# Kernel tuning notes

Measured on AMD Instinct MI355X. Metric: run time of the kernel, lower is better.

## Reference

```python
import jax, jax.numpy as jnp
import numpy as np

N_NODES = 50000
N_REL = 8
IN_DIM = 128
HID = 128
N_EDGES = 800000
N_TRIP = 100000


def setup_inputs() -> dict:
    key = jax.random.key(0)
    ks = jax.random.split(key, 12)
    s = 0.05
    return {
        "emb": jax.random.normal(ks[0], (N_NODES, IN_DIM), jnp.float32),
        "W0": jax.random.normal(ks[1], (N_REL, IN_DIM, HID), jnp.float32) * s,
        "root0": jax.random.normal(ks[2], (IN_DIM, HID), jnp.float32) * s,
        "b0": jnp.zeros((HID,), jnp.float32),
        "W1": jax.random.normal(ks[3], (N_REL, HID, HID), jnp.float32) * s,
        "root1": jax.random.normal(ks[4], (HID, HID), jnp.float32) * s,
        "b1": jnp.zeros((HID,), jnp.float32),
        "rel_emb": jax.random.normal(ks[5], (N_REL, HID), jnp.float32),
        "edge_index": jax.random.randint(ks[6], (2, N_EDGES), 0, N_NODES, jnp.int64 if jax.config.read('jax_enable_x64') else jnp.int32),
        "edge_type": jax.random.randint(ks[7], (N_EDGES,), 0, N_REL, jnp.int32),
        "head_idx": jax.random.randint(ks[8], (N_TRIP,), 0, N_NODES, jnp.int32),
        "rel_idx": jax.random.randint(ks[9], (N_TRIP,), 0, N_REL, jnp.int32),
        "tail_idx": jax.random.randint(ks[10], (N_TRIP,), 0, N_NODES, jnp.int32),
    }


def _rgcn_layer(h, W, root, bias, src, dst, edge_type):
    # PyG RGCNConv: per-relation MEAN aggregation of neighbor features at dst,
    # transformed by the relation weight, plus root transform and bias.
    # Mean commutes with the linear map, so aggregate raw features first.
    n, r = N_NODES, N_REL
    seg = dst * r + edge_type  # (E,) joint (dst, relation) segment id
    msg = h[src]               # (E, d) irregular gather
    sums = jax.ops.segment_sum(msg, seg, num_segments=n * r)          # (N*R, d)
    cnt = jax.ops.segment_sum(jnp.ones((src.shape[0],), h.dtype), seg,
                              num_segments=n * r)                     # (N*R,)
    mean = (sums / jnp.maximum(cnt, 1.0)[:, None]).reshape(n, r, -1)  # (N, R, d)
    return jnp.einsum('nrd,rdh->nh', mean, W) + h @ root + bias


def reference(emb, W0, root0, b0, W1, root1, b1, rel_emb,
              edge_index, edge_type, head_idx, rel_idx, tail_idx):
    src = edge_index[0]
    dst = edge_index[1]
    et = edge_type.astype(jnp.int32)
    h = emb
    h = jax.nn.relu(_rgcn_layer(h, W0, root0, b0, src, dst, et))
    h = jax.nn.relu(_rgcn_layer(h, W1, root1, b1, src, dst, et))
    # DistMult score: sum(h_head * r * h_tail)
    score = jnp.sum(h[head_idx] * rel_emb[rel_idx] * h[tail_idx], axis=-1)
    return score
```

## Files before the change

### kernel.cpp

```cpp
#include <hip/hip_runtime.h>
#include <hip/hip_bf16.h>

#define N_NODES 50000
#define N_REL   8
#define DIM     128
#define N_EDGES 800000
#define N_TRIP  100000
#define NDBLK   196
#define NB2     (N_REL * NDBLK)
#define CAP2    1024
#define NOFF    (N_REL * N_NODES + 1)

typedef __attribute__((ext_vector_type(8))) short bf16x8;
typedef __attribute__((ext_vector_type(4))) float f32x4;

static __device__ __forceinline__ unsigned short f2b(float f) {
    __hip_bfloat16 h = __float2bfloat16(f);
    return *reinterpret_cast<unsigned short*>(&h);
}
static __device__ __forceinline__ float blo(unsigned int u) {
    return __uint_as_float(u << 16);
}
static __device__ __forceinline__ float bhi(unsigned int u) {
    return __uint_as_float(u & 0xffff0000u);
}
static __device__ __forceinline__ int lds_off(int row, int chunk) {
    return (row * 16 + (chunk ^ (row & 7))) * 8;
}

__global__ __launch_bounds__(256) void bucket_scatter(
        const int* __restrict__ edge_index,
        const int* __restrict__ edge_type,
        int* __restrict__ gcnt,
        unsigned int* __restrict__ slack) {
    __shared__ int hist[NB2];
    __shared__ int cur[NB2];
    int tid = threadIdx.x;
    for (int i = tid; i < NB2; i += 256) hist[i] = 0;
    __syncthreads();
    int base = blockIdx.x * 4096;
    unsigned int w[16];
    int bk[16];
    #pragma unroll
    for (int i = 0; i < 16; ++i) {
        int e = base + i * 256 + tid;
        if (e < N_EDGES) {
            int src = edge_index[e];
            int dst = edge_index[N_EDGES + e];
            int r = edge_type[e];
            w[i] = (unsigned int)src | ((unsigned int)(dst & 255) << 16);
            bk[i] = r * NDBLK + (dst >> 8);
            atomicAdd(&hist[bk[i]], 1);
        } else {
            bk[i] = -1;
        }
    }
    __syncthreads();
    for (int i = tid; i < NB2; i += 256)
        cur[i] = atomicAdd(&gcnt[i], hist[i]);
    __syncthreads();
    #pragma unroll
    for (int i = 0; i < 16; ++i) {
        if (bk[i] >= 0) {
            int p = atomicAdd(&cur[bk[i]], 1);
            if (p < CAP2) slack[(size_t)bk[i] * CAP2 + p] = w[i];
        }
    }
}

__global__ void bucket_scan(const int* __restrict__ gcnt,
                            int* __restrict__ gbase,
                            int* __restrict__ offR) {
    __shared__ int sh[256];
    int t = threadIdx.x;
    int c[8];
    int s = 0;
    #pragma unroll
    for (int j = 0; j < 8; ++j) {
        int idx = t * 8 + j;
        int v = (idx < NB2) ? gcnt[idx] : 0;
        c[j] = v; s += v;
    }
    sh[t] = s;
    __syncthreads();
    #pragma unroll
    for (int off = 1; off < 256; off <<= 1) {
        int x = (t >= off) ? sh[t - off] : 0;
        __syncthreads();
        sh[t] += x;
        __syncthreads();
    }
    int ex = sh[t] - s;
    #pragma unroll
    for (int j = 0; j < 8; ++j) {
        int idx = t * 8 + j;
        if (idx < NB2) gbase[idx] = ex;
        ex += c[j];
    }
    if (t == 0) offR[N_REL * N_NODES] = N_EDGES;
}

__global__ __launch_bounds__(256) void bucket_sort(
        const unsigned int* __restrict__ slack,
        const int* __restrict__ gcnt,
        const int* __restrict__ gbase,
        unsigned int* __restrict__ spack,
        int* __restrict__ offR) {
    __shared__ unsigned int ebuf[CAP2];
    __shared__ unsigned int obuf[CAP2];
    __shared__ int hist[256];
    __shared__ int excl[256];
    __shared__ int sh[256];
    int b = blockIdx.x, t = threadIdx.x;
    int r = b / NDBLK, dblk = b % NDBLK;
    int n = gcnt[b]; if (n > CAP2) n = CAP2;
    int bb = gbase[b];
    for (int i = t; i < n; i += 256) ebuf[i] = slack[(size_t)b * CAP2 + i];
    hist[t] = 0;
    __syncthreads();
    for (int i = t; i < n; i += 256)
        atomicAdd(&hist[(ebuf[i] >> 16) & 255], 1);
    __syncthreads();
    int c = hist[t];
    sh[t] = c;
    __syncthreads();
    #pragma unroll
    for (int off = 1; off < 256; off <<= 1) {
        int x = (t >= off) ? sh[t - off] : 0;
        __syncthreads();
        sh[t] += x;
        __syncthreads();
    }
    int ex = sh[t] - c;
    excl[t] = ex;
    hist[t] = ex;
    __syncthreads();
    for (int i = t; i < n; i += 256) {
        unsigned int w = ebuf[i];
        int p = atomicAdd(&hist[(w >> 16) & 255], 1);
        obuf[p] = w;
    }
    __syncthreads();
    for (int i = t; i < n; i += 256) spack[bb + i] = obuf[i];
    int dst = dblk * 256 + t;
    if (dst < N_NODES) offR[r * N_NODES + dst] = bb + excl[t];
}

__global__ void cvt_emb_kernel(const float* __restrict__ src,
                               unsigned short* __restrict__ dst) {
    int i = blockIdx.x * blockDim.x + threadIdx.x;
    const int npair = N_NODES * DIM / 2;
    if (i >= npair) return;
    float2 v = ((const float2*)src)[i];
    unsigned int p = (unsigned int)f2b(v.x) | ((unsigned int)f2b(v.y) << 16);
    ((unsigned int*)dst)[i] = p;
}

__global__ void cvt_w2_kernel(const float* __restrict__ root0,
                              const float* __restrict__ W0,
                              const float* __restrict__ root1,
                              const float* __restrict__ W1,
                              unsigned short* __restrict__ Wt2a,
                              unsigned short* __restrict__ Wt2b) {
    int s = blockIdx.x;
    int n = blockIdx.y;
    int k = threadIdx.x;
    const float* root = blockIdx.z ? root1 : root0;
    const float* W    = blockIdx.z ? W1 : W0;
    unsigned short* Wt2 = blockIdx.z ? Wt2b : Wt2a;
    float v = (s == 0) ? root[k * 128 + n]
                       : W[((size_t)(s - 1) * 128 + k) * 128 + n];
    Wt2[((size_t)s * 128 + n) * 128 + k] = f2b(v);
}

__global__ __launch_bounds__(256) void rgcn_fused(
        const unsigned short* __restrict__ hb,
        const unsigned short* __restrict__ Wt2,
        const float* __restrict__ bias,
        const int* __restrict__ offR,
        const unsigned int* __restrict__ spack,
        unsigned short* __restrict__ hout) {
    __shared__ unsigned short Mbuf[64 * 16 * 8];
    unsigned int* Mb32 = (unsigned int*)Mbuf;
    const unsigned int* hb32 = (const unsigned int*)hb;

    int tid = threadIdx.x;
    int wid = tid >> 6, lane = tid & 63;
    int quad = lane >> 4, l16 = lane & 15;
    int t0 = blockIdx.x * 64;
    int col0w = wid * 32;

    f32x4 acc[4][2];
    #pragma unroll
    for (int mi = 0; mi < 4; ++mi)
        #pragma unroll
        for (int ni = 0; ni < 2; ++ni)
            acc[mi][ni] = (f32x4){0.f, 0.f, 0.f, 0.f};

    {
        const unsigned short* Wp = Wt2 + ((size_t)(col0w + l16)) * DIM + quad * 8;
        bf16x8 bf[2][4];
        #pragma unroll
        for (int ni = 0; ni < 2; ++ni)
            #pragma unroll
            for (int kk = 0; kk < 4; ++kk)
                bf[ni][kk] = *(const bf16x8*)(Wp + (ni * 16) * DIM + kk * 32);
        #pragma unroll
        for (int kk = 0; kk < 4; ++kk)
            #pragma unroll
            for (int mi = 0; mi < 4; ++mi) {
                int grow = t0 + mi * 16 + l16;
                if (grow >= N_NODES) grow = N_NODES - 1;
                bf16x8 af = *(const bf16x8*)(hb + (size_t)grow * DIM + kk * 32 + quad * 8);
                #pragma unroll
                for (int ni = 0; ni < 2; ++ni)
                    acc[mi][ni] = __builtin_amdgcn_mfma_f32_16x16x32_bf16(
                        af, bf[ni][kk], acc[mi][ni], 0, 0, 0);
            }
    }

    for (int r = 0; r < N_REL; ++r) {
        const unsigned short* Wp = Wt2 + ((size_t)(1 + r) * DIM + col0w + l16) * DIM + quad * 8;
        bf16x8 bf[2][4];
        #pragma unroll
        for (int ni = 0; ni < 2; ++ni)
            #pragma unroll
            for (int kk = 0; kk < 4; ++kk)
                bf[ni][kk] = *(const bf16x8*)(Wp + (ni * 16) * DIM + kk * 32);

        int d0 = t0 + wid * 16;
        int ia = d0 < N_NODES ? d0 : N_NODES;
        int ib = (d0 + 16) < N_NODES ? (d0 + 16) : N_NODES;
        int beg = offR[r * N_NODES + ia];
        int end = offR[r * N_NODES + ib];
        unsigned int flushed = 0;
        float a0 = 0.f, a1 = 0.f;
        int curd = -1, cnt = 0;
        for (int base = beg; base < end; base += 64) {
            int m = end - base; if (m > 64) m = 64;
            unsigned int pk = 0;
            if (lane < m) pk = spack[base + lane];
            for (int j = 0; j < m; j += 8) {
                int bc = m - j; if (bc > 8) bc = 8;
                unsigned int pp[8], vv[8];
                #pragma unroll
                for (int q = 0; q < 8; ++q)
                    if (q < bc) pp[q] = (unsigned int)__shfl((int)pk, j + q, 64);
                #pragma unroll
                for (int q = 0; q < 8; ++q)
                    if (q < bc) vv[q] = hb32[(size_t)(pp[q] & 0xffffu) * 64 + lane];
                #pragma unroll
                for (int q = 0; q < 8; ++q) {
                    if (q < bc) {
                        int dl = (int)((pp[q] >> 16) & 63u);
                        float x0 = blo(vv[q]), x1 = bhi(vv[q]);
                        if (dl != curd) {
                            if (curd >= 0) {
                                float inv = __builtin_amdgcn_rcpf((float)cnt);
                                Mb32[(curd * 16 + ((lane >> 2) ^ (curd & 7))) * 4 + (lane & 3)] =
                                    (unsigned int)f2b(a0 * inv) |
                                    ((unsigned int)f2b(a1 * inv) << 16);
                                flushed |= 1u << (curd & 15);
                            }
                            curd = dl; a0 = x0; a1 = x1; cnt = 1;
                        } else {
                            a0 += x0; a1 += x1; ++cnt;
                        }
                    }
                }
            }
        }
        if (curd >= 0) {
            float inv = __builtin_amdgcn_rcpf((float)cnt);
            Mb32[(curd * 16 + ((lane >> 2) ^ (curd & 7))) * 4 + (lane & 3)] =
                (unsigned int)f2b(a0 * inv) | ((unsigned int)f2b(a1 * inv) << 16);
            flushed |= 1u << (curd & 15);
        }
        #pragma unroll
        for (int i = 0; i < 16; ++i) {
            if (!((flushed >> i) & 1u)) {
                int row = wid * 16 + i;
                Mb32[(row * 16 + ((lane >> 2) ^ (row & 7))) * 4 + (lane & 3)] = 0u;
            }
        }
        __syncthreads();

        #pragma unroll
        for (int kk = 0; kk < 4; ++kk)
            #pragma unroll
            for (int mi = 0; mi < 4; ++mi) {
                bf16x8 af = *(const bf16x8*)&Mbuf[lds_off(mi * 16 + l16, kk * 4 + quad)];
                #pragma unroll
                for (int ni = 0; ni < 2; ++ni)
                    acc[mi][ni] = __builtin_amdgcn_mfma_f32_16x16x32_bf16(
                        af, bf[ni][kk], acc[mi][ni], 0, 0, 0);
            }
        __syncthreads();
    }

    #pragma unroll
    for (int ni = 0; ni < 2; ++ni) {
        int gc = col0w + ni * 16 + l16;
        float bv = bias[gc];
        #pragma unroll
        for (int mi = 0; mi < 4; ++mi)
            #pragma unroll
            for (int rr = 0; rr < 4; ++rr) {
                int grow = t0 + mi * 16 + quad * 4 + rr;
                if (grow < N_NODES)
                    hout[(size_t)grow * DIM + gc] = f2b(fmaxf(acc[mi][ni][rr] + bv, 0.f));
            }
    }
}

__global__ void score_kernel(const unsigned short* __restrict__ hb,
                             const float* __restrict__ rel_emb,
                             const int* __restrict__ head,
                             const int* __restrict__ rel,
                             const int* __restrict__ tail,
                             float* __restrict__ out) {
    int t = blockIdx.x * 4 + (threadIdx.x >> 6);
    if (t >= N_TRIP) return;
    int lane = threadIdx.x & 63;
    unsigned int ph = ((const unsigned int*)(hb + (size_t)head[t] * DIM))[lane];
    unsigned int pt = ((const unsigned int*)(hb + (size_t)tail[t] * DIM))[lane];
    float2 rr = ((const float2*)(rel_emb + (size_t)rel[t] * DIM))[lane];
    float s = blo(ph) * rr.x * blo(pt) + bhi(ph) * rr.y * bhi(pt);
    #pragma unroll
    for (int off = 32; off; off >>= 1) s += __shfl_xor(s, off, 64);
    if (lane == 0) out[t] = s;
}

extern "C" void kernel_launch(void* const* d_in, const int* in_sizes, int n_in,
                              void* d_out, int out_size, void* d_ws, size_t ws_size,
                              hipStream_t stream) {
    const float* emb     = (const float*)d_in[0];
    const float* W0      = (const float*)d_in[1];
    const float* root0   = (const float*)d_in[2];
    const float* b0      = (const float*)d_in[3];
    const float* W1      = (const float*)d_in[4];
    const float* root1   = (const float*)d_in[5];
    const float* b1      = (const float*)d_in[6];
    const float* rel_emb = (const float*)d_in[7];
    const int* edge_index = (const int*)d_in[8];
    const int* edge_type  = (const int*)d_in[9];
    const int* head_idx   = (const int*)d_in[10];
    const int* rel_idx    = (const int*)d_in[11];
    const int* tail_idx   = (const int*)d_in[12];
    float* out = (float*)d_out;

    char* p = (char*)d_ws;
    size_t hb_bytes  = (size_t)N_NODES * DIM * sizeof(unsigned short);
    size_t wt2_bytes = (size_t)9 * 128 * 128 * sizeof(unsigned short);
    unsigned short* embb = (unsigned short*)p; p += hb_bytes;
    unsigned short* h1b  = (unsigned short*)p; p += hb_bytes;
    unsigned short* h2b  = (unsigned short*)p; p += hb_bytes;
    unsigned short* Wt2a = (unsigned short*)p; p += wt2_bytes;
    unsigned short* Wt2b = (unsigned short*)p; p += wt2_bytes;
    unsigned int* spack = (unsigned int*)p;   p += (size_t)N_EDGES * sizeof(unsigned int);
    unsigned int* slack = (unsigned int*)p;   p += (size_t)NB2 * CAP2 * sizeof(unsigned int);
    int* gcnt  = (int*)p;  p += (size_t)NB2 * sizeof(int);
    int* gbase = (int*)p;  p += (size_t)NB2 * sizeof(int);
    int* offR  = (int*)p;  p += (size_t)NOFF * sizeof(int);
    (void)ws_size; (void)in_sizes; (void)n_in; (void)out_size;

    dim3 blk256(256);

    hipMemsetAsync(gcnt, 0, (size_t)NB2 * sizeof(int), stream);
    bucket_scatter<<<(N_EDGES + 4095) / 4096, blk256, 0, stream>>>(edge_index, edge_type,
                                                                   gcnt, slack);
    bucket_scan<<<1, 256, 0, stream>>>(gcnt, gbase, offR);
    bucket_sort<<<NB2, blk256, 0, stream>>>(slack, gcnt, gbase, spack, offR);

    cvt_emb_kernel<<<(N_NODES * DIM / 2 + 255) / 256, blk256, 0, stream>>>(emb, embb);
    cvt_w2_kernel<<<dim3(9, 128, 2), 128, 0, stream>>>(root0, W0, root1, W1, Wt2a, Wt2b);

    int fgrid = (N_NODES + 63) / 64;

    rgcn_fused<<<fgrid, blk256, 0, stream>>>(embb, Wt2a, b0, offR, spack, h1b);
    rgcn_fused<<<fgrid, blk256, 0, stream>>>(h1b, Wt2b, b1, offR, spack, h2b);

    score_kernel<<<(N_TRIP + 3) / 4, blk256, 0, stream>>>(h2b, rel_emb, head_idx, rel_idx,
                                                          tail_idx, out);
}
```

Measured before the change: 365.3 us.

## Halve node tile, double-buffer LDS, and prefetch per-relation edge offsets

Shrinks each block to 32 destination nodes (8 per wave) to double the grid, double-buffers the shared mean buffer so one barrier per relation suffices, and loads all relation offsets up front via lane shuffles while prefetching the next relation's edge packet. The gather loop splits into a full 8-wide unmasked path and a scalar tail. Smaller tiles mean weights are reloaded per relation for half as many rows, raising weight traffic.

```diff
diff --git a/kernel.cpp b/kernel.cpp
--- a/kernel.cpp
+++ b/kernel.cpp
@@ -9,7 +9,8 @@
 #define NDBLK   196
 #define NB2     (N_REL * NDBLK)
 #define CAP2    1024
-#define NOFF    (N_REL * N_NODES + 1)
+#define NSEG    (N_REL * N_NODES)
+#define NOFF    (NSEG + 1)
 
 typedef __attribute__((ext_vector_type(8))) short bf16x8;
 typedef __attribute__((ext_vector_type(4))) float f32x4;
@@ -97,7 +98,7 @@
         if (idx < NB2) gbase[idx] = ex;
         ex += c[j];
     }
-    if (t == 0) offR[N_REL * N_NODES] = N_EDGES;
+    if (t == 0) offR[NSEG] = N_EDGES;
 }
 
 __global__ __launch_bounds__(256) void bucket_sort(
@@ -173,6 +174,14 @@
     Wt2[((size_t)s * 128 + n) * 128 + k] = f2b(v);
 }
 
+#define FLUSH_ROW()                                                            \
+    do {                                                                       \
+        float inv_ = __builtin_amdgcn_rcpf((float)cnt);                        \
+        MbU[(curd * 16 + ((lane >> 2) ^ (curd & 7))) * 4 + (lane & 3)] =       \
+            (unsigned int)f2b(a0 * inv_) | ((unsigned int)f2b(a1 * inv_) << 16);\
+        flushed |= 1u << (curd & 7);                                           \
+    } while (0)
+
 __global__ __launch_bounds__(256) void rgcn_fused(
         const unsigned short* __restrict__ hb,
         const unsigned short* __restrict__ Wt2,
@@ -180,25 +189,32 @@
         const int* __restrict__ offR,
         const unsigned int* __restrict__ spack,
         unsigned short* __restrict__ hout) {
-    __shared__ unsigned short Mbuf[64 * 16 * 8];
-    unsigned int* Mb32 = (unsigned int*)Mbuf;
-    const unsigned int* hb32 = (const unsigned int*)hb;
+    __shared__ unsigned short Mbuf[2][32 * 16 * 8];
 
     int tid = threadIdx.x;
     int wid = tid >> 6, lane = tid & 63;
     int quad = lane >> 4, l16 = lane & 15;
-    int t0 = blockIdx.x * 64;
+    int t0 = blockIdx.x * 32;
     int col0w = wid * 32;
-
-    f32x4 acc[4][2];
-    #pragma unroll
-    for (int mi = 0; mi < 4; ++mi)
+    const unsigned int* hb32 = (const unsigned int*)hb;
+
+    int d0 = t0 + wid * 8;
+    int d0c = d0 < N_NODES ? d0 : N_NODES;
+    int d1c = (d0 + 8) < N_NODES ? (d0 + 8) : N_NODES;
+
+    int bb = 0;
+    if (lane < 16)
+        bb = offR[(size_t)(lane & 7) * N_NODES + ((lane < 8) ? d0c : d1c)];
+
+    f32x4 acc[2][2];
+    #pragma unroll
+    for (int mi = 0; mi < 2; ++mi)
         #pragma unroll
         for (int ni = 0; ni < 2; ++ni)
             acc[mi][ni] = (f32x4){0.f, 0.f, 0.f, 0.f};
 
     {
-        const unsigned short* Wp = Wt2 + ((size_t)(col0w + l16)) * DIM + quad * 8;
+        const unsigned short* Wp = Wt2 + (size_t)(col0w + l16) * DIM + quad * 8;
         bf16x8 bf[2][4];
         #pragma unroll
         for (int ni = 0; ni < 2; ++ni)
@@ -208,7 +224,7 @@
         #pragma unroll
         for (int kk = 0; kk < 4; ++kk)
             #pragma unroll
-            for (int mi = 0; mi < 4; ++mi) {
+            for (int mi = 0; mi < 2; ++mi) {
                 int grow = t0 + mi * 16 + l16;
                 if (grow >= N_NODES) grow = N_NODES - 1;
                 bf16x8 af = *(const bf16x8*)(hb + (size_t)grow * DIM + kk * 32 + quad * 8);
@@ -219,7 +235,18 @@
             }
     }
 
+    int beg_n = __shfl(bb, 0, 64);
+    int end_n = __shfl(bb, 8, 64);
+    unsigned int pk_n = 0;
+    {
+        int m0 = end_n - beg_n; if (m0 > 64) m0 = 64;
+        if (lane < m0) pk_n = spack[beg_n + lane];
+    }
+
     for (int r = 0; r < N_REL; ++r) {
+        unsigned short* Mb = Mbuf[r & 1];
+        unsigned int* MbU = (unsigned int*)Mb;
+
         const unsigned short* Wp = Wt2 + ((size_t)(1 + r) * DIM + col0w + l16) * DIM + quad * 8;
         bf16x8 bf[2][4];
         #pragma unroll
@@ -228,59 +255,62 @@
             for (int kk = 0; kk < 4; ++kk)
                 bf[ni][kk] = *(const bf16x8*)(Wp + (ni * 16) * DIM + kk * 32);
 
-        int d0 = t0 + wid * 16;
-        int ia = d0 < N_NODES ? d0 : N_NODES;
-        int ib = (d0 + 16) < N_NODES ? (d0 + 16) : N_NODES;
-        int beg = offR[r * N_NODES + ia];
-        int end = offR[r * N_NODES + ib];
-        unsigned int flushed = 0;
+        int beg = beg_n, end = end_n;
+        unsigned int pk = pk_n;
+        if (r < 7) {
+            beg_n = __shfl(bb, r + 1, 64);
+            end_n = __shfl(bb, 9 + r, 64);
+            int mn = end_n - beg_n; if (mn > 64) mn = 64;
+            pk_n = (lane < mn) ? spack[beg_n + lane] : 0;
+        }
+
         float a0 = 0.f, a1 = 0.f;
         int curd = -1, cnt = 0;
-        for (int base = beg; base < end; base += 64) {
+        unsigned int flushed = 0;
+        int base = beg;
+        while (base < end) {
             int m = end - base; if (m > 64) m = 64;
-            unsigned int pk = 0;
-            if (lane < m) pk = spack[base + lane];
-            for (int j = 0; j < m; j += 8) {
-                int bc = m - j; if (bc > 8) bc = 8;
+            int j = 0;
+            for (; j + 8 <= m; j += 8) {
                 unsigned int pp[8], vv[8];
                 #pragma unroll
                 for (int q = 0; q < 8; ++q)
-                    if (q < bc) pp[q] = (unsigned int)__shfl((int)pk, j + q, 64);
+                    pp[q] = (unsigned int)__shfl((int)pk, j + q, 64);
                 #pragma unroll
                 for (int q = 0; q < 8; ++q)
-                    if (q < bc) vv[q] = hb32[(size_t)(pp[q] & 0xffffu) * 64 + lane];
+                    vv[q] = hb32[(size_t)(pp[q] & 0xffffu) * 64 + lane];
                 #pragma unroll
                 for (int q = 0; q < 8; ++q) {
-                    if (q < bc) {
-                        int dl = (int)((pp[q] >> 16) & 63u);
-                        float x0 = blo(vv[q]), x1 = bhi(vv[q]);
-                        if (dl != curd) {
-                            if (curd >= 0) {
-                                float inv = __builtin_amdgcn_rcpf((float)cnt);
-                                Mb32[(curd * 16 + ((lane >> 2) ^ (curd & 7))) * 4 + (lane & 3)] =
-                                    (unsigned int)f2b(a0 * inv) |
-                                    ((unsigned int)f2b(a1 * inv) << 16);
-                                flushed |= 1u << (curd & 15);
-                            }
-                            curd = dl; a0 = x0; a1 = x1; cnt = 1;
-                        } else {
-                            a0 += x0; a1 += x1; ++cnt;
-                        }
-                    }
+                    int dl = (int)((pp[q] >> 16) & 31u);
+                    float x0 = blo(vv[q]), x1 = bhi(vv[q]);
+                    if (dl != curd) {
+                        if (curd >= 0) FLUSH_ROW();
+                        curd = dl; a0 = x0; a1 = x1; cnt = 1;
+                    } else { a0 += x0; a1 += x1; ++cnt; }
                 }
             }
+            for (; j < m; ++j) {
+                unsigned int p1 = (unsigned int)__shfl((int)pk, j, 64);
+                unsigned int v1 = hb32[(size_t)(p1 & 0xffffu) * 64 + lane];
+                int dl = (int)((p1 >> 16) & 31u);
+                float x0 = blo(v1), x1 = bhi(v1);
+                if (dl != curd) {
+                    if (curd >= 0) FLUSH_ROW();
+                    curd = dl; a0 = x0; a1 = x1; cnt = 1;
+                } else { a0 += x0; a1 += x1; ++cnt; }
+            }
+            base += 64;
+            if (base < end) {
+                int m2 = end - base; if (m2 > 64) m2 = 64;
+                pk = (lane < m2) ? spack[base + lane] : 0;
+            }
         }
-        if (curd >= 0) {
-            float inv = __builtin_amdgcn_rcpf((float)cnt);
-            Mb32[(curd * 16 + ((lane >> 2) ^ (curd & 7))) * 4 + (lane & 3)] =
-                (unsigned int)f2b(a0 * inv) | ((unsigned int)f2b(a1 * inv) << 16);
-            flushed |= 1u << (curd & 15);
-        }
-        #pragma unroll
-        for (int i = 0; i < 16; ++i) {
+        if (curd >= 0) FLUSH_ROW();
+        #pragma unroll
+        for (int i = 0; i < 8; ++i) {
             if (!((flushed >> i) & 1u)) {
-                int row = wid * 16 + i;
-                Mb32[(row * 16 + ((lane >> 2) ^ (row & 7))) * 4 + (lane & 3)] = 0u;
+                int row = wid * 8 + i;
+                MbU[(row * 16 + ((lane >> 2) ^ (row & 7))) * 4 + (lane & 3)] = 0u;
             }
         }
         __syncthreads();
@@ -288,14 +318,13 @@
         #pragma unroll
         for (int kk = 0; kk < 4; ++kk)
             #pragma unroll
-            for (int mi = 0; mi < 4; ++mi) {
-                bf16x8 af = *(const bf16x8*)&Mbuf[lds_off(mi * 16 + l16, kk * 4 + quad)];
+            for (int mi = 0; mi < 2; ++mi) {
+                bf16x8 af = *(const bf16x8*)&Mb[lds_off(mi * 16 + l16, kk * 4 + quad)];
                 #pragma unroll
                 for (int ni = 0; ni < 2; ++ni)
                     acc[mi][ni] = __builtin_amdgcn_mfma_f32_16x16x32_bf16(
                         af, bf[ni][kk], acc[mi][ni], 0, 0, 0);
             }
-        __syncthreads();
     }
 
     #pragma unroll
@@ -303,7 +332,7 @@
         int gc = col0w + ni * 16 + l16;
         float bv = bias[gc];
         #pragma unroll
-        for (int mi = 0; mi < 4; ++mi)
+        for (int mi = 0; mi < 2; ++mi)
             #pragma unroll
             for (int rr = 0; rr < 4; ++rr) {
                 int grow = t0 + mi * 16 + quad * 4 + rr;
@@ -375,7 +404,7 @@
     cvt_emb_kernel<<<(N_NODES * DIM / 2 + 255) / 256, blk256, 0, stream>>>(emb, embb);
     cvt_w2_kernel<<<dim3(9, 128, 2), 128, 0, stream>>>(root0, W0, root1, W1, Wt2a, Wt2b);
 
-    int fgrid = (N_NODES + 63) / 64;
+    int fgrid = (N_NODES + 31) / 32;
 
     rgcn_fused<<<fgrid, blk256, 0, stream>>>(embb, Wt2a, b0, offR, spack, h1b);
     rgcn_fused<<<fgrid, blk256, 0, stream>>>(h1b, Wt2b, b1, offR, spack, h2b);
```

Result: slower. 389.7 us (+6.7%).
